# Kernel optimization log

Hardware: AMD Instinct MI355X
Metric: run time of the kernel (lower is better)

## Reference

```python
import jax, jax.numpy as jnp
import numpy as np


def setup_inputs() -> dict:
    key = jax.random.key(0)
    ks = jax.random.split(key, 7)
    B, P, D = 32, 576, 768   # batch, tokens (24x24 patches), inp_dim
    H, HD = 12, 64           # n_heads, head_dim = inp_dim // n_heads
    s = 0.02
    return {
        "x": jax.random.normal(ks[0], (B, P, D), dtype=jnp.float32),
        "Wq": jax.random.normal(ks[1], (H, D, HD), dtype=jnp.float32) * s,
        "bq": jax.random.normal(ks[2], (H, HD), dtype=jnp.float32) * s,
        "Wk": jax.random.normal(ks[3], (H, D, HD), dtype=jnp.float32) * s,
        "bk": jax.random.normal(ks[4], (H, HD), dtype=jnp.float32) * s,
        "Wv": jax.random.normal(ks[5], (H, D, HD), dtype=jnp.float32) * s,
        "bv": jax.random.normal(ks[6], (H, HD), dtype=jnp.float32) * s,
    }


def reference(x, Wq, bq, Wk, bk, Wv, bv):
    # Per-head independent linear projections (stacked over head axis h).
    # x: [b, p, d]; Wq/Wk/Wv: [h, d, k]; biases: [h, k]
    q = jnp.einsum("bpd,hdk->bhpk", x, Wq) + bq[None, :, None, :]
    k = jnp.einsum("bpd,hdk->bhpk", x, Wk) + bk[None, :, None, :]
    v = jnp.einsum("bpd,hdk->bhpk", x, Wv) + bv[None, :, None, :]
    head_dim = k.shape[-1]
    scale = 1.0 / jnp.sqrt(jnp.asarray(head_dim, dtype=x.dtype))
    attn = jnp.einsum("bhqk,bhpk->bhqp", q, k) * scale  # [b, h, p, p]
    attn = jax.nn.softmax(attn, axis=-1)
    out = jnp.einsum("bhqp,bhpk->bhqk", attn, v)        # [b, h, p, k]
    b, h, p, hd = out.shape
    # concat heads along last dim (dropout is identity in eval mode)
    return jnp.transpose(out, (0, 2, 1, 3)).reshape(b, p, h * hd)
```

## Files before the change

### kernel.cpp

```cpp
#include <hip/hip_runtime.h>

typedef unsigned short ushort_t;
typedef unsigned int u32;
typedef float f32x4 __attribute__((ext_vector_type(4)));
typedef short short8 __attribute__((ext_vector_type(8)));

#define WT_BYTES  (36*64*768*2)
#define XB_BYTES  (32*576*768*2)
#define KV_BYTES  (32*12*576*64*2)
#define QSCALE    0.18033688f

static __device__ __forceinline__ ushort_t f2bf(float f) {
    return __builtin_bit_cast(ushort_t, (__bf16)f);
}
static __device__ __forceinline__ short8 pack8(float4 a, float4 b) {
    union { ushort_t u[8]; short8 v; } pk;
    pk.u[0]=f2bf(a.x); pk.u[1]=f2bf(a.y); pk.u[2]=f2bf(a.z); pk.u[3]=f2bf(a.w);
    pk.u[4]=f2bf(b.x); pk.u[5]=f2bf(b.y); pk.u[6]=f2bf(b.z); pk.u[7]=f2bf(b.w);
    return pk.v;
}
static __device__ __forceinline__ void gl_lds16(const ushort_t* g, ushort_t* l) {
    __builtin_amdgcn_global_load_lds((const __attribute__((address_space(1))) u32*)g,
                                     (__attribute__((address_space(3))) u32*)l, 16, 0, 0);
}
static __device__ __forceinline__ int swzb(int row, int chunk) {
    return row * 128 + (((chunk ^ (row & 7)) & 7) << 4);
}
#define MFMA16 __builtin_amdgcn_mfma_f32_16x16x32_bf16

__global__ __launch_bounds__(256) void prep(
    const float* __restrict__ Wq, const float* __restrict__ Wk,
    const float* __restrict__ Wv, const float* __restrict__ x,
    ushort_t* __restrict__ Wt, ushort_t* __restrict__ xb)
{
    int idx = blockIdx.x * 256 + threadIdx.x;
    if (idx < 221184) {
        int d0   = (idx % 96) * 8;
        int rest = idx / 96;
        int hd   = rest & 63;
        int ph   = rest >> 6;
        int h    = ph % 12, pr = ph / 12;
        const float* W = (pr == 0) ? Wq : (pr == 1 ? Wk : Wv);
        union { ushort_t u[8]; short8 v; } pk;
        #pragma unroll
        for (int j = 0; j < 8; ++j)
            pk.u[j] = f2bf(W[(size_t)(h * 768 + d0 + j) * 64 + hd]);
        *(short8*)(Wt + ((size_t)(ph * 64 + hd)) * 768 + d0) = pk.v;
    } else {
        size_t e = (size_t)(idx - 221184) * 8;
        const float4* xp = (const float4*)(x + e);
        *(short8*)(xb + e) = pack8(xp[0], xp[1]);
    }
}

__global__ __launch_bounds__(256) void proj_kv(
    const ushort_t* __restrict__ xb, const ushort_t* __restrict__ Wt,
    const float* __restrict__ bk, const float* __restrict__ bv,
    ushort_t* __restrict__ Kb, ushort_t* __restrict__ Vtb)
{
    __shared__ ushort_t smem[18432];

    const int t = threadIdx.x;
    const int w = t >> 6, l = t & 63, m16 = l & 15, g = l >> 4;
    const int wm = w >> 1, wn = w & 1;

    int L = blockIdx.y * 12 + blockIdx.x;
    int xcd = L & 7, jj_ = L >> 3;
    int nt = jj_ % 12, mt = (jj_ / 12) * 8 + xcd;
    const int m0 = mt * 128;
    const int ph0 = 12 + nt * 2;

    const int grow = l >> 3, gch = (l & 7) ^ grow;

    auto stageA = [&](int kc) {
        #pragma unroll
        for (int c4 = 0; c4 < 4; ++c4) {
            int ci = w * 4 + c4;
            gl_lds16(xb + (size_t)(m0 + ci * 8 + grow) * 768 + kc * 64 + gch * 8,
                     smem + ci * 512);
        }
    };
    auto stageB = [&](int kc) {
        #pragma unroll
        for (int c4 = 0; c4 < 4; ++c4) {
            int ci = w * 4 + c4;
            int r  = ci * 8 + grow;
            gl_lds16(Wt + ((size_t)(ph0 + (r >> 6)) * 64 + (r & 63)) * 768 + kc * 64 + gch * 8,
                     smem + 8192 + ci * 512);
        }
    };

    f32x4 acc[4][4] = {};

    for (int kc = 0; kc < 12; ++kc) {
        __syncthreads();
        stageA(kc); stageB(kc);
        __syncthreads();
        __builtin_amdgcn_s_setprio(1);
        #pragma unroll
        for (int jj = 0; jj < 2; ++jj) {
            short8 af[4], bf[4];
            #pragma unroll
            for (int mi = 0; mi < 4; ++mi)
                af[mi] = *(const short8*)((char*)smem + swzb(wm * 64 + mi * 16 + m16, jj * 4 + g));
            #pragma unroll
            for (int ni = 0; ni < 4; ++ni)
                bf[ni] = *(const short8*)((char*)smem + 16384 + swzb(wn * 64 + ni * 16 + m16, jj * 4 + g));
            #pragma unroll
            for (int mi = 0; mi < 4; ++mi)
                #pragma unroll
                for (int ni = 0; ni < 4; ++ni)
                    acc[mi][ni] = MFMA16(af[mi], bf[ni], acc[mi][ni], 0, 0, 0);
        }
        __builtin_amdgcn_s_setprio(0);
    }
    __syncthreads();

    const int ph = ph0 + wn, proj = ph / 12, h = ph % 12;
    const float* bias = (proj == 1 ? bk : bv) + h * 64;
    const int tokg0 = m0 + wm * 64;
    const int bb = tokg0 / 576, pp = tokg0 % 576;
    ushort_t* sE = smem + w * 4608;

    #pragma unroll
    for (int ni = 0; ni < 4; ++ni) {
        float bvv = bias[ni * 16 + m16];
        #pragma unroll
        for (int mi = 0; mi < 4; ++mi)
            #pragma unroll
            for (int i = 0; i < 4; ++i) {
                float val = acc[mi][ni][i] + bvv;
                int tok = mi * 16 + g * 4 + i;
                int hd  = ni * 16 + m16;
                if (proj == 1) sE[tok * 72 + hd] = f2bf(val);
                else           sE[hd * 72 + tok] = f2bf(val);
            }
    }
    if (proj == 1) {
        ushort_t* dst = Kb + ((size_t)(bb * 12 + h) * 576 + pp) * 64;
        #pragma unroll
        for (int rr = 0; rr < 8; ++rr) {
            int row = rr * 8 + (l >> 3), ch = l & 7;
            *(short8*)(dst + (size_t)row * 64 + ch * 8) = *(const short8*)&sE[row * 72 + ch * 8];
        }
    } else {
        ushort_t* dst = Vtb + (size_t)(bb * 12 + h) * 64 * 576 + pp;
        #pragma unroll
        for (int rr = 0; rr < 8; ++rr) {
            int hd = rr * 8 + (l >> 3), tc = l & 7;
            *(short8*)(dst + (size_t)hd * 576 + tc * 8) = *(const short8*)&sE[hd * 72 + tc * 8];
        }
    }
}

__global__ __launch_bounds__(256) void proj_reg(
    const float* __restrict__ x, const ushort_t* __restrict__ Wt,
    const float* __restrict__ bk, const float* __restrict__ bv,
    ushort_t* __restrict__ Kb, ushort_t* __restrict__ Vtb)
{
    __shared__ ushort_t smem[22528];

    const int t = threadIdx.x;
    const int w = t >> 6, l = t & 63, m16 = l & 15, g = l >> 4;
    const int wm = w >> 1, wn = w & 1;

    int L = blockIdx.y * 12 + blockIdx.x;
    int xcd = L & 7, jj_ = L >> 3;
    int nt = jj_ % 12, mt = (jj_ / 12) * 8 + xcd;
    const int m0 = mt * 96;
    const int b  = mt / 6, pb = (mt % 6) * 96;

    const int grow = l >> 3, gch = (l & 7) ^ grow;

    float4 ar[3][2];
    auto loadA = [&](int kc) {
        #pragma unroll
        for (int q = 0; q < 3; ++q) {
            int c = t + q * 256, row = c >> 3, ch = c & 7;
            const float4* xp = (const float4*)(x + (size_t)(m0 + row) * 768 + kc * 64 + ch * 8);
            ar[q][0] = xp[0]; ar[q][1] = xp[1];
        }
    };
    auto writeA = [&]() {
        #pragma unroll
        for (int q = 0; q < 3; ++q) {
            int c = t + q * 256, row = c >> 3, ch = c & 7;
            *(short8*)((char*)smem + swzb(row, ch)) = pack8(ar[q][0], ar[q][1]);
        }
    };
    auto stageB = [&](int kc, int d) {
        #pragma unroll
        for (int c4 = 0; c4 < 4; ++c4) {
            int ci = w * 4 + c4;
            const ushort_t* gs = Wt + (size_t)((12 + nt * 2) * 64 + ci * 8 + grow) * 768
                               + kc * 64 + gch * 8;
            gl_lds16(gs, smem + 6144 + d * 8192 + ci * 512);
        }
    };

    f32x4 acc[3][4] = {};
    loadA(0); stageB(0, 0); writeA();
    __syncthreads();

    for (int kc = 0; kc < 12; ++kc) {
        const int d = kc & 1;
        if (kc < 11) { loadA(kc + 1); stageB(kc + 1, d ^ 1); }
        __builtin_amdgcn_s_setprio(1);
        #pragma unroll
        for (int jj = 0; jj < 2; ++jj) {
            short8 af[3], bf[4];
            #pragma unroll
            for (int mi = 0; mi < 3; ++mi)
                af[mi] = *(const short8*)((char*)smem + swzb(wm * 48 + mi * 16 + m16, jj * 4 + g));
            #pragma unroll
            for (int ni = 0; ni < 4; ++ni)
                bf[ni] = *(const short8*)((char*)smem + 12288 + d * 16384 + swzb(wn * 64 + ni * 16 + m16, jj * 4 + g));
            #pragma unroll
            for (int mi = 0; mi < 3; ++mi)
                #pragma unroll
                for (int ni = 0; ni < 4; ++ni)
                    acc[mi][ni] = MFMA16(af[mi], bf[ni], acc[mi][ni], 0, 0, 0);
        }
        __builtin_amdgcn_s_setprio(0);
        __syncthreads();
        if (kc < 11) { writeA(); __syncthreads(); }
    }

    const int ph = 12 + nt * 2 + wn;
    const int proj = ph / 12, h = ph % 12;
    const float* bias = (proj == 1 ? bk : bv) + h * 64;
    ushort_t* sE = smem + w * 4608;

    #pragma unroll
    for (int ni = 0; ni < 4; ++ni) {
        float bvv = bias[ni * 16 + m16];
        #pragma unroll
        for (int mi = 0; mi < 3; ++mi)
            #pragma unroll
            for (int i = 0; i < 4; ++i) {
                float val = acc[mi][ni][i] + bvv;
                int tok = mi * 16 + g * 4 + i;
                int hd  = ni * 16 + m16;
                if (proj == 1) sE[tok * 72 + hd] = f2bf(val);
                else           sE[hd * 72 + tok] = f2bf(val);
            }
    }
    if (proj == 1) {
        ushort_t* dst = Kb + ((size_t)(b * 12 + h) * 576 + pb + wm * 48) * 64;
        #pragma unroll
        for (int rr = 0; rr < 6; ++rr) {
            int row = rr * 8 + (l >> 3), ch = l & 7;
            *(short8*)(dst + (size_t)row * 64 + ch * 8) = *(const short8*)&sE[row * 72 + ch * 8];
        }
    } else {
        ushort_t* dst = Vtb + (size_t)(b * 12 + h) * 64 * 576 + pb + wm * 48;
        #pragma unroll
        for (int rr = 0; rr < 8; ++rr) {
            int hd = rr * 8 + (l >> 3), tc = l & 7;
            if (tc < 6)
                *(short8*)(dst + (size_t)hd * 576 + tc * 8) = *(const short8*)&sE[hd * 72 + tc * 8];
        }
    }
}

template<int MODE>
__global__ __launch_bounds__(256) void attn_k(
    const float* __restrict__ x, const ushort_t* __restrict__ xb,
    const ushort_t* __restrict__ Wt, const float* __restrict__ bq,
    const ushort_t* __restrict__ Kb, const ushort_t* __restrict__ Vtb,
    float* __restrict__ out)
{
    __shared__ ushort_t smem[20480];

    const int t = threadIdx.x;
    const int w = t >> 6, l = t & 63, m16 = l & 15, g = l >> 4;

    int L = blockIdx.y * 9 + blockIdx.x;
    int xcd = L & 7, jj_ = L >> 3;
    int qt = jj_ % 9, bh = (jj_ / 9) * 8 + xcd;
    const int b = bh / 12, h = bh % 12;
    const int p0 = qt * 64;

    const int grow = l >> 3, gch = (l & 7) ^ grow;
    const int spbase = 32768 + w * 2048;

    short8 aq0, aq1;
    {
        f32x4 acc[4] = {};
        auto stage = [&](int kc, int d) {
            if constexpr (MODE == 2) {
                #pragma unroll
                for (int c2 = 0; c2 < 2; ++c2) {
                    int ci = w * 2 + c2;
                    gl_lds16(xb + (size_t)(b * 576 + p0 + ci * 8 + grow) * 768 + kc * 64 + gch * 8,
                             smem + (d * 8192 + ci * 1024) / 2);
                    gl_lds16(Wt + (size_t)(h * 64 + ci * 8 + grow) * 768 + kc * 64 + gch * 8,
                             smem + (16384 + d * 8192 + ci * 1024) / 2);
                }
            } else {
                const int row = t >> 2, c16 = (t & 3) * 16;
                const float4* xp = (const float4*)(x + (size_t)(b * 576 + p0 + row) * 768 + kc * 64 + c16);
                float4 u0 = xp[0], u1 = xp[1], u2 = xp[2], u3 = xp[3];
                *(short8*)((char*)smem + d * 8192 + swzb(row, c16 >> 3))       = pack8(u0, u1);
                *(short8*)((char*)smem + d * 8192 + swzb(row, (c16 >> 3) + 1)) = pack8(u2, u3);
                #pragma unroll
                for (int c2 = 0; c2 < 2; ++c2) {
                    int ci = w * 2 + c2;
                    gl_lds16(Wt + (size_t)(h * 64 + ci * 8 + grow) * 768 + kc * 64 + gch * 8,
                             smem + (16384 + d * 8192 + ci * 1024) / 2);
                }
            }
        };
        stage(0, 0); __syncthreads();
        for (int kc = 0; kc < 12; ++kc) {
            int d = kc & 1;
            if (kc < 11) stage(kc + 1, d ^ 1);
            __builtin_amdgcn_s_setprio(1);
            #pragma unroll
            for (int jj = 0; jj < 2; ++jj) {
                short8 a = *(const short8*)((char*)smem + d * 8192 + swzb(w * 16 + m16, jj * 4 + g));
                #pragma unroll
                for (int f = 0; f < 4; ++f) {
                    short8 bb = *(const short8*)((char*)smem + 16384 + d * 8192 + swzb(f * 16 + m16, jj * 4 + g));
                    acc[f] = MFMA16(a, bb, acc[f], 0, 0, 0);
                }
            }
            __builtin_amdgcn_s_setprio(0);
            __syncthreads();
        }
        #pragma unroll
        for (int f = 0; f < 4; ++f) {
            float bqv = bq[h * 64 + f * 16 + m16];
            #pragma unroll
            for (int i = 0; i < 4; ++i) {
                float val = (acc[f][i] + bqv) * QSCALE;
                int r = g * 4 + i, c = f * 16 + m16;
                *(ushort_t*)((char*)smem + spbase + r * 128
                    + (((((c >> 3) ^ (r & 7)) & 7) << 4) | ((c & 7) << 1))) = f2bf(val);
            }
        }
        aq0 = *(const short8*)((char*)smem + spbase + m16 * 128 + (((g ^ (m16 & 7)) & 7) << 4));
        aq1 = *(const short8*)((char*)smem + spbase + m16 * 128 + ((((4 + g) ^ (m16 & 7)) & 7) << 4));
    }

    const ushort_t* Kbase = Kb  + (size_t)bh * (576 * 64);
    const ushort_t* Vbase = Vtb + (size_t)bh * (64 * 576);

    auto stageKV = [&](int kt, int d) {
        #pragma unroll
        for (int c2 = 0; c2 < 2; ++c2) {
            int ci = w * 2 + c2;
            gl_lds16(Kbase + (size_t)(kt * 64 + ci * 8 + grow) * 64 + gch * 8,
                     smem + (d * 8192 + ci * 1024) / 2);
            gl_lds16(Vbase + (size_t)(ci * 8 + grow) * 576 + kt * 64 + gch * 8,
                     smem + (16384 + d * 8192 + ci * 1024) / 2);
        }
    };

    float psum[4] = {0.f, 0.f, 0.f, 0.f};
    f32x4 accO[4] = {};

    stageKV(0, 0); __syncthreads();
    for (int kt = 0; kt < 9; ++kt) {
        int d = kt & 1;
        if (kt < 8) stageKV(kt + 1, d ^ 1);

        f32x4 s[4] = {};
        __builtin_amdgcn_s_setprio(1);
        #pragma unroll
        for (int jj = 0; jj < 2; ++jj) {
            short8 aqj = jj ? aq1 : aq0;
            #pragma unroll
            for (int f = 0; f < 4; ++f) {
                short8 bk_ = *(const short8*)((char*)smem + d * 8192 + swzb(f * 16 + m16, jj * 4 + g));
                s[f] = MFMA16(aqj, bk_, s[f], 0, 0, 0);
            }
        }
        __builtin_amdgcn_s_setprio(0);

        #pragma unroll
        for (int f = 0; f < 4; ++f)
            #pragma unroll
            for (int i = 0; i < 4; ++i) {
                float p = exp2f(s[f][i]);
                s[f][i] = p;
                psum[i] += p;
            }

        #pragma unroll
        for (int f = 0; f < 4; ++f)
            #pragma unroll
            for (int i = 0; i < 4; ++i) {
                int r = g * 4 + i, c = f * 16 + m16;
                *(ushort_t*)((char*)smem + spbase + r * 128
                    + (((((c >> 3) ^ (r & 7)) & 7) << 4) | ((c & 7) << 1))) = f2bf(s[f][i]);
            }
        short8 pa0 = *(const short8*)((char*)smem + spbase + m16 * 128 + (((g ^ (m16 & 7)) & 7) << 4));
        short8 pa1 = *(const short8*)((char*)smem + spbase + m16 * 128 + ((((4 + g) ^ (m16 & 7)) & 7) << 4));

        __builtin_amdgcn_s_setprio(1);
        #pragma unroll
        for (int jj = 0; jj < 2; ++jj) {
            short8 paj = jj ? pa1 : pa0;
            #pragma unroll
            for (int f = 0; f < 4; ++f) {
                short8 bv_ = *(const short8*)((char*)smem + 16384 + d * 8192 + swzb(f * 16 + m16, jj * 4 + g));
                accO[f] = MFMA16(paj, bv_, accO[f], 0, 0, 0);
            }
        }
        __builtin_amdgcn_s_setprio(0);
        __syncthreads();
    }

    #pragma unroll
    for (int xm = 1; xm < 16; xm <<= 1)
        #pragma unroll
        for (int i = 0; i < 4; ++i)
            psum[i] += __shfl_xor(psum[i], xm, 64);

    float inv[4];
    #pragma unroll
    for (int i = 0; i < 4; ++i) inv[i] = 1.0f / psum[i];
    float* orow = out + ((size_t)b * 576 + p0 + w * 16) * 768 + h * 64;
    #pragma unroll
    for (int f = 0; f < 4; ++f)
        #pragma unroll
        for (int i = 0; i < 4; ++i)
            orow[(size_t)(g * 4 + i) * 768 + f * 16 + m16] = accO[f][i] * inv[i];
}

extern "C" void kernel_launch(void* const* d_in, const int* in_sizes, int n_in,
                              void* d_out, int out_size, void* d_ws, size_t ws_size,
                              hipStream_t stream) {
    const float* x  = (const float*)d_in[0];
    const float* Wq = (const float*)d_in[1];
    const float* bq = (const float*)d_in[2];
    const float* Wk = (const float*)d_in[3];
    const float* bk = (const float*)d_in[4];
    const float* Wv = (const float*)d_in[5];
    const float* bv = (const float*)d_in[6];
    float* out = (float*)d_out;

    const bool bigws = ws_size >= (size_t)WT_BYTES + XB_BYTES + 2 * (size_t)KV_BYTES;

    if (bigws) {
        ushort_t* Wt  = (ushort_t*)d_ws;
        ushort_t* xbp = (ushort_t*)((char*)d_ws + WT_BYTES);
        ushort_t* Kb  = (ushort_t*)((char*)d_ws + WT_BYTES + XB_BYTES);
        ushort_t* Vtb = (ushort_t*)((char*)d_ws + WT_BYTES + XB_BYTES + (size_t)KV_BYTES);
        hipLaunchKernelGGL(prep, dim3(7776), dim3(256), 0, stream, Wq, Wk, Wv, x, Wt, xbp);
        hipLaunchKernelGGL(proj_kv, dim3(12, 144), dim3(256), 0, stream,
                           xbp, Wt, bk, bv, Kb, Vtb);
        hipLaunchKernelGGL((attn_k<2>), dim3(9, 384), dim3(256), 0, stream,
                           x, xbp, Wt, bq, Kb, Vtb, out);
    } else {
        ushort_t* Wt  = (ushort_t*)d_ws;
        ushort_t* Kb  = (ushort_t*)((char*)d_ws + WT_BYTES);
        ushort_t* Vtb = (ushort_t*)((char*)d_ws + WT_BYTES + (size_t)KV_BYTES);
        hipLaunchKernelGGL(prep, dim3(864), dim3(256), 0, stream, Wq, Wk, Wv, x, Wt, (ushort_t*)nullptr);
        hipLaunchKernelGGL(proj_reg, dim3(12, 192), dim3(256), 0, stream,
                           x, Wt, bk, bv, Kb, Vtb);
        hipLaunchKernelGGL((attn_k<1>), dim3(9, 384), dim3(256), 0, stream,
                           x, (const ushort_t*)nullptr, Wt, bq, Kb, Vtb, out);
    }
}
```

Before: 180.9 us.

## Move Q projection into batched proj GEMM and single-buffer V in attention

Q is now computed in the projection GEMM alongside K and V (grid widened to 18 column tiles, with bias and softmax scale folded in) and written as bf16 to workspace, so the attention kernel loads Q directly instead of recomputing it per query tile. The attention loop stages V separately into a single buffer, using an explicit vmcnt wait and barrier before the PV MFMAs, which shrinks LDS to 32KB. The row-sum accumulation is vectorised. This adds a Q round-trip through global memory and needs a larger workspace.

```diff
diff --git a/kernel.cpp b/kernel.cpp
--- a/kernel.cpp
+++ b/kernel.cpp
@@ -6,7 +6,6 @@
 typedef short short8 __attribute__((ext_vector_type(8)));
 
 #define WT_BYTES  (36*64*768*2)
-#define XB_BYTES  (32*576*768*2)
 #define KV_BYTES  (32*12*576*64*2)
 #define QSCALE    0.18033688f
 
@@ -55,8 +54,10 @@
 
 __global__ __launch_bounds__(256) void proj_kv(
     const ushort_t* __restrict__ xb, const ushort_t* __restrict__ Wt,
-    const float* __restrict__ bk, const float* __restrict__ bv,
-    ushort_t* __restrict__ Kb, ushort_t* __restrict__ Vtb)
+    const float* __restrict__ bq, const float* __restrict__ bk,
+    const float* __restrict__ bv,
+    ushort_t* __restrict__ Qb, ushort_t* __restrict__ Kb,
+    ushort_t* __restrict__ Vtb, int nts, int ph_base)
 {
     __shared__ ushort_t smem[18432];
 
@@ -64,11 +65,11 @@
     const int w = t >> 6, l = t & 63, m16 = l & 15, g = l >> 4;
     const int wm = w >> 1, wn = w & 1;
 
-    int L = blockIdx.y * 12 + blockIdx.x;
+    int L = blockIdx.y * gridDim.x + blockIdx.x;
     int xcd = L & 7, jj_ = L >> 3;
-    int nt = jj_ % 12, mt = (jj_ / 12) * 8 + xcd;
+    int nt = jj_ % nts, mt = (jj_ / nts) * 8 + xcd;
     const int m0 = mt * 128;
-    const int ph0 = 12 + nt * 2;
+    const int ph0 = ph_base + nt * 2;
 
     const int grow = l >> 3, gch = (l & 7) ^ grow;
 
@@ -117,7 +118,8 @@
     __syncthreads();
 
     const int ph = ph0 + wn, proj = ph / 12, h = ph % 12;
-    const float* bias = (proj == 1 ? bk : bv) + h * 64;
+    const float* bias = (proj == 0 ? bq : (proj == 1 ? bk : bv)) + h * 64;
+    const float qs = (proj == 0) ? QSCALE : 1.0f;
     const int tokg0 = m0 + wm * 64;
     const int bb = tokg0 / 576, pp = tokg0 % 576;
     ushort_t* sE = smem + w * 4608;
@@ -127,6 +129,115 @@
         float bvv = bias[ni * 16 + m16];
         #pragma unroll
         for (int mi = 0; mi < 4; ++mi)
+            #pragma unroll
+            for (int i = 0; i < 4; ++i) {
+                float val = (acc[mi][ni][i] + bvv) * qs;
+                int tok = mi * 16 + g * 4 + i;
+                int hd  = ni * 16 + m16;
+                if (proj < 2) sE[tok * 72 + hd] = f2bf(val);
+                else          sE[hd * 72 + tok] = f2bf(val);
+            }
+    }
+    if (proj < 2) {
+        ushort_t* dst = (proj == 0 ? Qb : Kb) + ((size_t)(bb * 12 + h) * 576 + pp) * 64;
+        #pragma unroll
+        for (int rr = 0; rr < 8; ++rr) {
+            int row = rr * 8 + (l >> 3), ch = l & 7;
+            *(short8*)(dst + (size_t)row * 64 + ch * 8) = *(const short8*)&sE[row * 72 + ch * 8];
+        }
+    } else {
+        ushort_t* dst = Vtb + (size_t)(bb * 12 + h) * 64 * 576 + pp;
+        #pragma unroll
+        for (int rr = 0; rr < 8; ++rr) {
+            int hd = rr * 8 + (l >> 3), tc = l & 7;
+            *(short8*)(dst + (size_t)hd * 576 + tc * 8) = *(const short8*)&sE[hd * 72 + tc * 8];
+        }
+    }
+}
+
+__global__ __launch_bounds__(256) void proj_reg(
+    const float* __restrict__ x, const ushort_t* __restrict__ Wt,
+    const float* __restrict__ bk, const float* __restrict__ bv,
+    ushort_t* __restrict__ Kb, ushort_t* __restrict__ Vtb)
+{
+    __shared__ ushort_t smem[22528];
+
+    const int t = threadIdx.x;
+    const int w = t >> 6, l = t & 63, m16 = l & 15, g = l >> 4;
+    const int wm = w >> 1, wn = w & 1;
+
+    int L = blockIdx.y * 12 + blockIdx.x;
+    int xcd = L & 7, jj_ = L >> 3;
+    int nt = jj_ % 12, mt = (jj_ / 12) * 8 + xcd;
+    const int m0 = mt * 96;
+    const int b  = mt / 6, pb = (mt % 6) * 96;
+
+    const int grow = l >> 3, gch = (l & 7) ^ grow;
+
+    float4 ar[3][2];
+    auto loadA = [&](int kc) {
+        #pragma unroll
+        for (int q = 0; q < 3; ++q) {
+            int c = t + q * 256, row = c >> 3, ch = c & 7;
+            const float4* xp = (const float4*)(x + (size_t)(m0 + row) * 768 + kc * 64 + ch * 8);
+            ar[q][0] = xp[0]; ar[q][1] = xp[1];
+        }
+    };
+    auto writeA = [&]() {
+        #pragma unroll
+        for (int q = 0; q < 3; ++q) {
+            int c = t + q * 256, row = c >> 3, ch = c & 7;
+            *(short8*)((char*)smem + swzb(row, ch)) = pack8(ar[q][0], ar[q][1]);
+        }
+    };
+    auto stageB = [&](int kc, int d) {
+        #pragma unroll
+        for (int c4 = 0; c4 < 4; ++c4) {
+            int ci = w * 4 + c4;
+            const ushort_t* gs = Wt + (size_t)((12 + nt * 2) * 64 + ci * 8 + grow) * 768
+                               + kc * 64 + gch * 8;
+            gl_lds16(gs, smem + 6144 + d * 8192 + ci * 512);
+        }
+    };
+
+    f32x4 acc[3][4] = {};
+    loadA(0); stageB(0, 0); writeA();
+    __syncthreads();
+
+    for (int kc = 0; kc < 12; ++kc) {
+        const int d = kc & 1;
+        if (kc < 11) { loadA(kc + 1); stageB(kc + 1, d ^ 1); }
+        __builtin_amdgcn_s_setprio(1);
+        #pragma unroll
+        for (int jj = 0; jj < 2; ++jj) {
+            short8 af[3], bf[4];
+            #pragma unroll
+            for (int mi = 0; mi < 3; ++mi)
+                af[mi] = *(const short8*)((char*)smem + swzb(wm * 48 + mi * 16 + m16, jj * 4 + g));
+            #pragma unroll
+            for (int ni = 0; ni < 4; ++ni)
+                bf[ni] = *(const short8*)((char*)smem + 12288 + d * 16384 + swzb(wn * 64 + ni * 16 + m16, jj * 4 + g));
+            #pragma unroll
+            for (int mi = 0; mi < 3; ++mi)
+                #pragma unroll
+                for (int ni = 0; ni < 4; ++ni)
+                    acc[mi][ni] = MFMA16(af[mi], bf[ni], acc[mi][ni], 0, 0, 0);
+        }
+        __builtin_amdgcn_s_setprio(0);
+        __syncthreads();
+        if (kc < 11) { writeA(); __syncthreads(); }
+    }
+
+    const int ph = 12 + nt * 2 + wn;
+    const int proj = ph / 12, h = ph % 12;
+    const float* bias = (proj == 1 ? bk : bv) + h * 64;
+    ushort_t* sE = smem + w * 4608;
+
+    #pragma unroll
+    for (int ni = 0; ni < 4; ++ni) {
+        float bvv = bias[ni * 16 + m16];
+        #pragma unroll
+        for (int mi = 0; mi < 3; ++mi)
             #pragma unroll
             for (int i = 0; i < 4; ++i) {
                 float val = acc[mi][ni][i] + bvv;
@@ -137,115 +248,6 @@
             }
     }
     if (proj == 1) {
-        ushort_t* dst = Kb + ((size_t)(bb * 12 + h) * 576 + pp) * 64;
-        #pragma unroll
-        for (int rr = 0; rr < 8; ++rr) {
-            int row = rr * 8 + (l >> 3), ch = l & 7;
-            *(short8*)(dst + (size_t)row * 64 + ch * 8) = *(const short8*)&sE[row * 72 + ch * 8];
-        }
-    } else {
-        ushort_t* dst = Vtb + (size_t)(bb * 12 + h) * 64 * 576 + pp;
-        #pragma unroll
-        for (int rr = 0; rr < 8; ++rr) {
-            int hd = rr * 8 + (l >> 3), tc = l & 7;
-            *(short8*)(dst + (size_t)hd * 576 + tc * 8) = *(const short8*)&sE[hd * 72 + tc * 8];
-        }
-    }
-}
-
-__global__ __launch_bounds__(256) void proj_reg(
-    const float* __restrict__ x, const ushort_t* __restrict__ Wt,
-    const float* __restrict__ bk, const float* __restrict__ bv,
-    ushort_t* __restrict__ Kb, ushort_t* __restrict__ Vtb)
-{
-    __shared__ ushort_t smem[22528];
-
-    const int t = threadIdx.x;
-    const int w = t >> 6, l = t & 63, m16 = l & 15, g = l >> 4;
-    const int wm = w >> 1, wn = w & 1;
-
-    int L = blockIdx.y * 12 + blockIdx.x;
-    int xcd = L & 7, jj_ = L >> 3;
-    int nt = jj_ % 12, mt = (jj_ / 12) * 8 + xcd;
-    const int m0 = mt * 96;
-    const int b  = mt / 6, pb = (mt % 6) * 96;
-
-    const int grow = l >> 3, gch = (l & 7) ^ grow;
-
-    float4 ar[3][2];
-    auto loadA = [&](int kc) {
-        #pragma unroll
-        for (int q = 0; q < 3; ++q) {
-            int c = t + q * 256, row = c >> 3, ch = c & 7;
-            const float4* xp = (const float4*)(x + (size_t)(m0 + row) * 768 + kc * 64 + ch * 8);
-            ar[q][0] = xp[0]; ar[q][1] = xp[1];
-        }
-    };
-    auto writeA = [&]() {
-        #pragma unroll
-        for (int q = 0; q < 3; ++q) {
-            int c = t + q * 256, row = c >> 3, ch = c & 7;
-            *(short8*)((char*)smem + swzb(row, ch)) = pack8(ar[q][0], ar[q][1]);
-        }
-    };
-    auto stageB = [&](int kc, int d) {
-        #pragma unroll
-        for (int c4 = 0; c4 < 4; ++c4) {
-            int ci = w * 4 + c4;
-            const ushort_t* gs = Wt + (size_t)((12 + nt * 2) * 64 + ci * 8 + grow) * 768
-                               + kc * 64 + gch * 8;
-            gl_lds16(gs, smem + 6144 + d * 8192 + ci * 512);
-        }
-    };
-
-    f32x4 acc[3][4] = {};
-    loadA(0); stageB(0, 0); writeA();
-    __syncthreads();
-
-    for (int kc = 0; kc < 12; ++kc) {
-        const int d = kc & 1;
-        if (kc < 11) { loadA(kc + 1); stageB(kc + 1, d ^ 1); }
-        __builtin_amdgcn_s_setprio(1);
-        #pragma unroll
-        for (int jj = 0; jj < 2; ++jj) {
-            short8 af[3], bf[4];
-            #pragma unroll
-            for (int mi = 0; mi < 3; ++mi)
-                af[mi] = *(const short8*)((char*)smem + swzb(wm * 48 + mi * 16 + m16, jj * 4 + g));
-            #pragma unroll
-            for (int ni = 0; ni < 4; ++ni)
-                bf[ni] = *(const short8*)((char*)smem + 12288 + d * 16384 + swzb(wn * 64 + ni * 16 + m16, jj * 4 + g));
-            #pragma unroll
-            for (int mi = 0; mi < 3; ++mi)
-                #pragma unroll
-                for (int ni = 0; ni < 4; ++ni)
-                    acc[mi][ni] = MFMA16(af[mi], bf[ni], acc[mi][ni], 0, 0, 0);
-        }
-        __builtin_amdgcn_s_setprio(0);
-        __syncthreads();
-        if (kc < 11) { writeA(); __syncthreads(); }
-    }
-
-    const int ph = 12 + nt * 2 + wn;
-    const int proj = ph / 12, h = ph % 12;
-    const float* bias = (proj == 1 ? bk : bv) + h * 64;
-    ushort_t* sE = smem + w * 4608;
-
-    #pragma unroll
-    for (int ni = 0; ni < 4; ++ni) {
-        float bvv = bias[ni * 16 + m16];
-        #pragma unroll
-        for (int mi = 0; mi < 3; ++mi)
-            #pragma unroll
-            for (int i = 0; i < 4; ++i) {
-                float val = acc[mi][ni][i] + bvv;
-                int tok = mi * 16 + g * 4 + i;
-                int hd  = ni * 16 + m16;
-                if (proj == 1) sE[tok * 72 + hd] = f2bf(val);
-                else           sE[hd * 72 + tok] = f2bf(val);
-            }
-    }
-    if (proj == 1) {
         ushort_t* dst = Kb + ((size_t)(b * 12 + h) * 576 + pb + wm * 48) * 64;
         #pragma unroll
         for (int rr = 0; rr < 6; ++rr) {
@@ -267,10 +269,10 @@
 __global__ __launch_bounds__(256) void attn_k(
     const float* __restrict__ x, const ushort_t* __restrict__ xb,
     const ushort_t* __restrict__ Wt, const float* __restrict__ bq,
-    const ushort_t* __restrict__ Kb, const ushort_t* __restrict__ Vtb,
-    float* __restrict__ out)
+    const ushort_t* __restrict__ Qb, const ushort_t* __restrict__ Kb,
+    const ushort_t* __restrict__ Vtb, float* __restrict__ out)
 {
-    __shared__ ushort_t smem[20480];
+    __shared__ ushort_t smem[16384];
 
     const int t = threadIdx.x;
     const int w = t >> 6, l = t & 63, m16 = l & 15, g = l >> 4;
@@ -282,12 +284,18 @@
     const int p0 = qt * 64;
 
     const int grow = l >> 3, gch = (l & 7) ^ grow;
-    const int spbase = 32768 + w * 2048;
+    const int spbase = 24576 + w * 2048;
 
     short8 aq0, aq1;
-    {
+
+    if constexpr (MODE == 3) {
+        const ushort_t* qsrc = Qb + ((size_t)bh * 576 + p0 + w * 16 + m16) * 64 + g * 8;
+        aq0 = *(const short8*)qsrc;
+        aq1 = *(const short8*)(qsrc + 32);
+    } else {
         f32x4 acc[4] = {};
         auto stage = [&](int kc, int d) {
+            const int boff = d ? 24576 : 16384;
             if constexpr (MODE == 2) {
                 #pragma unroll
                 for (int c2 = 0; c2 < 2; ++c2) {
@@ -295,7 +303,7 @@
                     gl_lds16(xb + (size_t)(b * 576 + p0 + ci * 8 + grow) * 768 + kc * 64 + gch * 8,
                              smem + (d * 8192 + ci * 1024) / 2);
                     gl_lds16(Wt + (size_t)(h * 64 + ci * 8 + grow) * 768 + kc * 64 + gch * 8,
-                             smem + (16384 + d * 8192 + ci * 1024) / 2);
+                             smem + (boff + ci * 1024) / 2);
                 }
             } else {
                 const int row = t >> 2, c16 = (t & 3) * 16;
@@ -307,13 +315,14 @@
                 for (int c2 = 0; c2 < 2; ++c2) {
                     int ci = w * 2 + c2;
                     gl_lds16(Wt + (size_t)(h * 64 + ci * 8 + grow) * 768 + kc * 64 + gch * 8,
-                             smem + (16384 + d * 8192 + ci * 1024) / 2);
+                             smem + (boff + ci * 1024) / 2);
                 }
             }
         };
         stage(0, 0); __syncthreads();
         for (int kc = 0; kc < 12; ++kc) {
             int d = kc & 1;
+            const int boff = d ? 24576 : 16384;
             if (kc < 11) stage(kc + 1, d ^ 1);
             __builtin_amdgcn_s_setprio(1);
             #pragma unroll
@@ -321,7 +330,7 @@
                 short8 a = *(const short8*)((char*)smem + d * 8192 + swzb(w * 16 + m16, jj * 4 + g));
                 #pragma unroll
                 for (int f = 0; f < 4; ++f) {
-                    short8 bb = *(const short8*)((char*)smem + 16384 + d * 8192 + swzb(f * 16 + m16, jj * 4 + g));
+                    short8 bb = *(const short8*)((char*)smem + boff + swzb(f * 16 + m16, jj * 4 + g));
                     acc[f] = MFMA16(a, bb, acc[f], 0, 0, 0);
                 }
             }
@@ -341,29 +350,37 @@
         }
         aq0 = *(const short8*)((char*)smem + spbase + m16 * 128 + (((g ^ (m16 & 7)) & 7) << 4));
         aq1 = *(const short8*)((char*)smem + spbase + m16 * 128 + ((((4 + g) ^ (m16 & 7)) & 7) << 4));
+        __syncthreads();
     }
 
     const ushort_t* Kbase = Kb  + (size_t)bh * (576 * 64);
     const ushort_t* Vbase = Vtb + (size_t)bh * (64 * 576);
 
-    auto stageKV = [&](int kt, int d) {
+    auto stageK = [&](int kt, int d) {
         #pragma unroll
         for (int c2 = 0; c2 < 2; ++c2) {
             int ci = w * 2 + c2;
             gl_lds16(Kbase + (size_t)(kt * 64 + ci * 8 + grow) * 64 + gch * 8,
                      smem + (d * 8192 + ci * 1024) / 2);
+        }
+    };
+    auto stageV = [&](int kt) {
+        #pragma unroll
+        for (int c2 = 0; c2 < 2; ++c2) {
+            int ci = w * 2 + c2;
             gl_lds16(Vbase + (size_t)(ci * 8 + grow) * 576 + kt * 64 + gch * 8,
-                     smem + (16384 + d * 8192 + ci * 1024) / 2);
-        }
-    };
-
-    float psum[4] = {0.f, 0.f, 0.f, 0.f};
+                     smem + (16384 + ci * 1024) / 2);
+        }
+    };
+
+    f32x4 psumv = {};
     f32x4 accO[4] = {};
 
-    stageKV(0, 0); __syncthreads();
+    stageK(0, 0); __syncthreads();
     for (int kt = 0; kt < 9; ++kt) {
         int d = kt & 1;
-        if (kt < 8) stageKV(kt + 1, d ^ 1);
+        stageV(kt);
+        if (kt < 8) stageK(kt + 1, d ^ 1);
 
         f32x4 s[4] = {};
         __builtin_amdgcn_s_setprio(1);
@@ -379,13 +396,12 @@
         __builtin_amdgcn_s_setprio(0);
 
         #pragma unroll
-        for (int f = 0; f < 4; ++f)
-            #pragma unroll
-            for (int i = 0; i < 4; ++i) {
-                float p = exp2f(s[f][i]);
-                s[f][i] = p;
-                psum[i] += p;
-            }
+        for (int f = 0; f < 4; ++f) {
+            #pragma unroll
+            for (int i = 0; i < 4; ++i)
+                s[f][i] = exp2f(s[f][i]);
+            psumv += s[f];
+        }
 
         #pragma unroll
         for (int f = 0; f < 4; ++f)
@@ -398,13 +414,18 @@
         short8 pa0 = *(const short8*)((char*)smem + spbase + m16 * 128 + (((g ^ (m16 & 7)) & 7) << 4));
         short8 pa1 = *(const short8*)((char*)smem + spbase + m16 * 128 + ((((4 + g) ^ (m16 & 7)) & 7) << 4));
 
+        if (kt < 8) asm volatile("s_waitcnt vmcnt(2)" ::: "memory");
+        else        asm volatile("s_waitcnt vmcnt(0)" ::: "memory");
+        __builtin_amdgcn_s_barrier();
+        __builtin_amdgcn_sched_barrier(0);
+
         __builtin_amdgcn_s_setprio(1);
         #pragma unroll
         for (int jj = 0; jj < 2; ++jj) {
             short8 paj = jj ? pa1 : pa0;
             #pragma unroll
             for (int f = 0; f < 4; ++f) {
-                short8 bv_ = *(const short8*)((char*)smem + 16384 + d * 8192 + swzb(f * 16 + m16, jj * 4 + g));
+                short8 bv_ = *(const short8*)((char*)smem + 16384 + swzb(f * 16 + m16, jj * 4 + g));
                 accO[f] = MFMA16(paj, bv_, accO[f], 0, 0, 0);
             }
         }
@@ -412,6 +433,9 @@
         __syncthreads();
     }
 
+    float psum[4];
+    #pragma unroll
+    for (int i = 0; i < 4; ++i) psum[i] = psumv[i];
     #pragma unroll
     for (int xm = 1; xm < 16; xm <<= 1)
         #pragma unroll
@@ -441,18 +465,30 @@
     const float* bv = (const float*)d_in[6];
     float* out = (float*)d_out;
 
-    const bool bigws = ws_size >= (size_t)WT_BYTES + XB_BYTES + 2 * (size_t)KV_BYTES;
-
-    if (bigws) {
+    const size_t T3 = (size_t)WT_BYTES + 4 * (size_t)KV_BYTES;
+    const size_t T2 = (size_t)WT_BYTES + 3 * (size_t)KV_BYTES;
+
+    if (ws_size >= T3) {
         ushort_t* Wt  = (ushort_t*)d_ws;
         ushort_t* xbp = (ushort_t*)((char*)d_ws + WT_BYTES);
-        ushort_t* Kb  = (ushort_t*)((char*)d_ws + WT_BYTES + XB_BYTES);
-        ushort_t* Vtb = (ushort_t*)((char*)d_ws + WT_BYTES + XB_BYTES + (size_t)KV_BYTES);
+        ushort_t* Qb  = (ushort_t*)((char*)d_ws + WT_BYTES + (size_t)KV_BYTES);
+        ushort_t* Kb  = (ushort_t*)((char*)d_ws + WT_BYTES + 2 * (size_t)KV_BYTES);
+        ushort_t* Vtb = (ushort_t*)((char*)d_ws + WT_BYTES + 3 * (size_t)KV_BYTES);
+        hipLaunchKernelGGL(prep, dim3(7776), dim3(256), 0, stream, Wq, Wk, Wv, x, Wt, xbp);
+        hipLaunchKernelGGL(proj_kv, dim3(18, 144), dim3(256), 0, stream,
+                           xbp, Wt, bq, bk, bv, Qb, Kb, Vtb, 18, 0);
+        hipLaunchKernelGGL((attn_k<3>), dim3(9, 384), dim3(256), 0, stream,
+                           x, xbp, Wt, bq, Qb, Kb, Vtb, out);
+    } else if (ws_size >= T2) {
+        ushort_t* Wt  = (ushort_t*)d_ws;
+        ushort_t* xbp = (ushort_t*)((char*)d_ws + WT_BYTES);
+        ushort_t* Kb  = (ushort_t*)((char*)d_ws + WT_BYTES + (size_t)KV_BYTES);
+        ushort_t* Vtb = (ushort_t*)((char*)d_ws + WT_BYTES + 2 * (size_t)KV_BYTES);
         hipLaunchKernelGGL(prep, dim3(7776), dim3(256), 0, stream, Wq, Wk, Wv, x, Wt, xbp);
         hipLaunchKernelGGL(proj_kv, dim3(12, 144), dim3(256), 0, stream,
-                           xbp, Wt, bk, bv, Kb, Vtb);
+                           xbp, Wt, bq, bk, bv, (ushort_t*)nullptr, Kb, Vtb, 12, 12);
         hipLaunchKernelGGL((attn_k<2>), dim3(9, 384), dim3(256), 0, stream,
-                           x, xbp, Wt, bq, Kb, Vtb, out);
+                           x, xbp, Wt, bq, (const ushort_t*)nullptr, Kb, Vtb, out);
     } else {
         ushort_t* Wt  = (ushort_t*)d_ws;
         ushort_t* Kb  = (ushort_t*)((char*)d_ws + WT_BYTES);
@@ -461,6 +497,6 @@
         hipLaunchKernelGGL(proj_reg, dim3(12, 192), dim3(256), 0, stream,
                            x, Wt, bk, bv, Kb, Vtb);
         hipLaunchKernelGGL((attn_k<1>), dim3(9, 384), dim3(256), 0, stream,
-                           x, (const ushort_t*)nullptr, Wt, bq, Kb, Vtb, out);
-    }
-}
+                           x, (const ushort_t*)nullptr, Wt, bq, (const ushort_t*)nullptr, Kb, Vtb, out);
+    }
+}
```

Result: no change. 180.9 us (-0.0%).
